# Optimization experiments

Measured on AMD Instinct MI355X. Metric: run time of the kernel, lower is better.

Reference implementation:

```python
import math
import jax, jax.numpy as jnp
import numpy as np

B, N, D, H, NI, NL, NS, MID = 32, 2048, 256, 8, 64, 3, 32, 3


def _ln(x, g, b, eps=1e-5):
    m = jnp.mean(x, axis=-1, keepdims=True)
    v = jnp.mean((x - m) ** 2, axis=-1, keepdims=True)
    return (x - m) * jax.lax.rsqrt(v + eps) * g + b


def _mab(Q, K, mask, Wq, bq, Wk, bk, Wv, bv, Wo, bo, g0, b0, g1, b1):
    # torch's split(dim_split,2)+cat(...,0) == reshape to (B, n, H, dh)
    dh = D // H
    q = (Q @ Wq + bq).reshape(Q.shape[0], Q.shape[1], H, dh)
    k = (K @ Wk + bk).reshape(K.shape[0], K.shape[1], H, dh)
    v = (K @ Wv + bv).reshape(K.shape[0], K.shape[1], H, dh)
    A = jnp.einsum('bqhd,bkhd->bhqk', q, k) / math.sqrt(D)  # note: sqrt(dim_V), faithful
    A = jnp.where(mask[:, None, None, :] == 0, -1e4, A)
    A = jax.nn.softmax(A, axis=-1)
    o = q + jnp.einsum('bhqk,bkhd->bqhd', A, v)
    O = o.reshape(Q.shape[0], Q.shape[1], D)
    O = _ln(O, g0, b0)
    O = O + jax.nn.relu(O @ Wo + bo)
    return _ln(O, g1, b1)


def _forward(x_values, y_target, point_mask, proj_W, proj_b, isab_I,
             isab_Wq, isab_bq, isab_Wk, isab_bk, isab_Wv, isab_bv,
             isab_Wo, isab_bo, isab_g0, isab_b0, isab_g1, isab_b1,
             pma_S, pma_Wq, pma_bq, pma_Wk, pma_bk, pma_Wv, pma_bv,
             pma_Wo, pma_bo, pma_g0, pma_b0, pma_g1, pma_b1):
    # input_dim == max_input_dim, so the zero-padded feature build is a concat
    feats = jnp.concatenate([x_values, y_target[..., None]], axis=-1)  # (B, N, MID+1)
    x = jax.nn.gelu(feats @ proj_W + proj_b, approximate=False)
    ones_mask = jnp.ones((x.shape[0], NI), jnp.float32)
    stk = (isab_Wq, isab_bq, isab_Wk, isab_bk, isab_Wv, isab_bv,
           isab_Wo, isab_bo, isab_g0, isab_b0, isab_g1, isab_b1)
    for l in range(NL):
        I = jnp.broadcast_to(isab_I[l][None], (x.shape[0], NI, D))
        h = _mab(I, x, point_mask, *[a[l, 0] for a in stk])   # mab0: inducing pts attend to X
        x = _mab(x, h, ones_mask, *[a[l, 1] for a in stk])    # mab1: X attends to H (all valid)
    S = jnp.broadcast_to(pma_S[None], (x.shape[0], NS, D))
    return _mab(S, x, point_mask, pma_Wq, pma_bq, pma_Wk, pma_bk, pma_Wv,
                pma_bv, pma_Wo, pma_bo, pma_g0, pma_b0, pma_g1, pma_b1)


def setup_inputs():
    key = jax.random.key(0)
    ks = iter(jax.random.split(key, 40))
    def nrm(shape, s=0.05):
        return jax.random.normal(next(ks), shape, dtype=jnp.float32) * s
    z = lambda shape: jnp.zeros(shape, jnp.float32)
    o = lambda shape: jnp.ones(shape, jnp.float32)
    return {
        'x_values': jax.random.normal(next(ks), (B, N, MID), jnp.float32),
        'y_target': jax.random.normal(next(ks), (B, N), jnp.float32),
        'point_mask': jax.random.randint(next(ks), (B, N), 0, 2).astype(jnp.float32),
        'proj_W': nrm((MID + 1, D)), 'proj_b': z((D,)),
        'isab_I': nrm((NL, NI, D), 0.1),
        'isab_Wq': nrm((NL, 2, D, D)), 'isab_bq': z((NL, 2, D)),
        'isab_Wk': nrm((NL, 2, D, D)), 'isab_bk': z((NL, 2, D)),
        'isab_Wv': nrm((NL, 2, D, D)), 'isab_bv': z((NL, 2, D)),
        'isab_Wo': nrm((NL, 2, D, D)), 'isab_bo': z((NL, 2, D)),
        'isab_g0': o((NL, 2, D)), 'isab_b0': z((NL, 2, D)),
        'isab_g1': o((NL, 2, D)), 'isab_b1': z((NL, 2, D)),
        'pma_S': nrm((NS, D), 0.1),
        'pma_Wq': nrm((D, D)), 'pma_bq': z((D,)),
        'pma_Wk': nrm((D, D)), 'pma_bk': z((D,)),
        'pma_Wv': nrm((D, D)), 'pma_bv': z((D,)),
        'pma_Wo': nrm((D, D)), 'pma_bo': z((D,)),
        'pma_g0': o((D,)), 'pma_b0': z((D,)),
        'pma_g1': o((D,)), 'pma_b1': z((D,)),
    }


def reference(x_values, y_target, point_mask, proj_W, proj_b, isab_I,
              isab_Wq, isab_bq, isab_Wk, isab_bk, isab_Wv, isab_bv,
              isab_Wo, isab_bo, isab_g0, isab_b0, isab_g1, isab_b1,
              pma_S, pma_Wq, pma_bq, pma_Wk, pma_bk, pma_Wv, pma_bv,
              pma_Wo, pma_bo, pma_g0, pma_b0, pma_g1, pma_b1):
    return _forward(x_values, y_target, point_mask, proj_W, proj_b, isab_I,
                    isab_Wq, isab_bq, isab_Wk, isab_bk, isab_Wv, isab_bv,
                    isab_Wo, isab_bo, isab_g0, isab_b0, isab_g1, isab_b1,
                    pma_S, pma_Wq, pma_bq, pma_Wk, pma_bk, pma_Wv, pma_bv,
                    pma_Wo, pma_bo, pma_g0, pma_b0, pma_g1, pma_b1)
```

## Files before the change

### kernel.cpp

```cpp
#include <hip/hip_runtime.h>
#include <hip/hip_bf16.h>


typedef __attribute__((ext_vector_type(8))) short short8;
typedef __attribute__((ext_vector_type(4))) float f32x4;
typedef __attribute__((ext_vector_type(4))) ushort ushort4v;

__device__ __forceinline__ ushort f2bf(float f) {
  uint u = __builtin_bit_cast(uint, f);
  u += 0x7fffu + ((u >> 16) & 1u);
  return (ushort)(u >> 16);
}
__device__ __forceinline__ float bf2f(ushort h) {
  uint u = (uint)h << 16;
  return __builtin_bit_cast(float, u);
}

__global__ __launch_bounds__(256) void prep_weights(
    const float* __restrict__ Wq, const float* __restrict__ Wk,
    const float* __restrict__ Wv, const float* __restrict__ Wo,
    const float* __restrict__ pWq, const float* __restrict__ pWk,
    const float* __restrict__ pWv, const float* __restrict__ pWo,
    ushort* __restrict__ wt)
{
  __shared__ float tile[64][65];
  const int m = blockIdx.y;
  const int t = blockIdx.x;
  const int tr = (t >> 2) * 64;
  const int tc = (t & 3) * 64;
  const float* src;
  if (m < 24) {
    int l = m >> 3, s = (m >> 2) & 1, w = m & 3;
    const float* base = (w == 0) ? Wq : (w == 1) ? Wk : (w == 2) ? Wv : Wo;
    src = base + (size_t)(l * 2 + s) * 65536;
  } else {
    int w = m & 3;
    src = (w == 0) ? pWq : (w == 1) ? pWk : (w == 2) ? pWv : pWo;
  }
  const int tid = threadIdx.x;
  const int cn = tid & 63;
  const int rk = tid >> 6;
#pragma unroll
  for (int j = 0; j < 16; ++j) {
    int kl = rk + j * 4;
    tile[kl][cn] = src[(size_t)(tr + kl) * 256 + tc + cn];
  }
  __syncthreads();
  ushort* dst = wt + (size_t)m * 65536;
#pragma unroll
  for (int j = 0; j < 16; ++j) {
    int nl = rk + j * 4;
    dst[(size_t)(tc + nl) * 256 + tr + cn] = f2bf(tile[cn][nl]);
  }
}

__global__ __launch_bounds__(256) void proj_gelu(
    const float* __restrict__ xv, const float* __restrict__ yt,
    const float* __restrict__ pW, const float* __restrict__ pb,
    ushort* __restrict__ xb)
{
  const int d = threadIdx.x;
  const int row0 = blockIdx.x * 8;
  const float w0 = pW[d], w1 = pW[256 + d], w2 = pW[512 + d], w3 = pW[768 + d];
  const float bz = pb[d];
#pragma unroll
  for (int rr = 0; rr < 8; ++rr) {
    int row = row0 + rr;
    float f0 = xv[(size_t)row * 3 + 0];
    float f1 = xv[(size_t)row * 3 + 1];
    float f2 = xv[(size_t)row * 3 + 2];
    float f3 = yt[row];
    float a = bz + f0 * w0 + f1 * w1 + f2 * w2 + f3 * w3;
    float g = 0.5f * a * (1.f + erff(a * 0.70710678118654752f));
    xb[(size_t)row * 256 + d] = f2bf(g);
  }
}

__global__ __launch_bounds__(256) void gemm_q(
    const float* __restrict__ iI, const float* __restrict__ pS,
    const ushort* __restrict__ wt, const float* __restrict__ ibq,
    const float* __restrict__ pbq, ushort* __restrict__ q_all)
{
  const int bq = blockIdx.x;
  const float* A; const ushort* Wt; const float* bias; ushort* out; int M;
  if (bq < 3) { A = iI + bq * 16384; Wt = wt + (size_t)(bq * 8) * 65536; bias = ibq + bq * 512; out = q_all + bq * 16384; M = 64; }
  else        { A = pS; Wt = wt + (size_t)24 * 65536; bias = pbq; out = q_all + 49152; M = 32; }
  const int tid = threadIdx.x;
  const int wave = tid >> 6, lane = tid & 63;
  const int l15 = lane & 15, l4 = lane >> 4, koff = l4 * 8;
  f32x4 acc[4][4];
#pragma unroll
  for (int i = 0; i < 4; ++i)
#pragma unroll
    for (int j = 0; j < 4; ++j) acc[i][j] = (f32x4)0.f;
#pragma unroll
  for (int ks = 0; ks < 8; ++ks) {
    short8 af[4];
#pragma unroll
    for (int mf = 0; mf < 4; ++mf) {
      if (mf * 16 < M) {
        const float* ap = A + (size_t)(mf * 16 + l15) * 256 + ks * 32 + koff;
        float4 f0 = *(const float4*)ap;
        float4 f1 = *(const float4*)(ap + 4);
        short8 sv;
        sv[0] = (short)f2bf(f0.x); sv[1] = (short)f2bf(f0.y);
        sv[2] = (short)f2bf(f0.z); sv[3] = (short)f2bf(f0.w);
        sv[4] = (short)f2bf(f1.x); sv[5] = (short)f2bf(f1.y);
        sv[6] = (short)f2bf(f1.z); sv[7] = (short)f2bf(f1.w);
        af[mf] = sv;
      } else af[mf] = (short8)0;
    }
#pragma unroll
    for (int nf = 0; nf < 4; ++nf) {
      short8 bf = *(const short8*)(Wt + (size_t)(wave * 64 + nf * 16 + l15) * 256 + ks * 32 + koff);
#pragma unroll
      for (int mf = 0; mf < 4; ++mf)
        acc[mf][nf] = __builtin_amdgcn_mfma_f32_16x16x32_bf16(af[mf], bf, acc[mf][nf], 0, 0, 0);
    }
  }
#pragma unroll
  for (int mf = 0; mf < 4; ++mf) {
    if (mf * 16 >= M) continue;
#pragma unroll
    for (int nf = 0; nf < 4; ++nf) {
      int col = wave * 64 + nf * 16 + l15;
      float bcol = bias[col];
#pragma unroll
      for (int r = 0; r < 4; ++r)
        out[(size_t)(mf * 16 + l4 * 4 + r) * 256 + col] = f2bf(acc[mf][nf][r] + bcol);
    }
  }
}

template <int EPI, bool OUTF32, int COLS>
__global__ __launch_bounds__(COLS * 2, (COLS == 128) ? 4 : 2) void gemm_bp(
    const ushort* __restrict__ A,
    const ushort* __restrict__ Wt0, const ushort* __restrict__ Wt1, const ushort* __restrict__ Wt2,
    const float* __restrict__ b0, const float* __restrict__ b1, const float* __restrict__ b2,
    void* __restrict__ o0, void* __restrict__ o1, void* __restrict__ o2,
    const float* __restrict__ lng, const float* __restrict__ lnb,
    int ny, int nyz)
{
  constexpr int WC = COLS / 64;
  constexpr int PS = COLS * 64;
  constexpr int ROWB = COLS * 2;
  __shared__ __align__(16) char Bs[4 * PS];
  __shared__ float redbuf[(EPI == 3) ? 1280 : 4];
  const int bid = blockIdx.x;
  const int rest = bid >> 3;
  const int yz = rest % nyz;
  const int bx = ((rest / nyz) << 3) | (bid & 7);
  const int y = yz % ny;
  const int z = yz / ny;
  const ushort* Wt = (z == 0) ? Wt0 : ((z == 1) ? Wt1 : Wt2);
  const float* bias = (z == 0) ? b0 : ((z == 1) ? b1 : b2);
  void* outp = (z == 0) ? o0 : ((z == 1) ? o1 : o2);
  const int pcol = y * COLS;

  const int tid = threadIdx.x;
  const int wave = tid >> 6, lane = tid & 63;
  const int wc = wave % WC, wr = wave / WC;
  const int l15 = lane & 15, l4 = lane >> 4;
  const int row0 = bx * 128;
  const int sn = tid >> 1, sseg = tid & 1;

  f32x4 acc[4][4];
#pragma unroll
  for (int i = 0; i < 4; ++i)
#pragma unroll
    for (int j = 0; j < 4; ++j) acc[i][j] = (f32x4)0.f;

#pragma unroll
  for (int half = 0; half < 2; ++half) {
    if (half) __syncthreads();
    {
      const ushort* src = Wt + (size_t)(pcol + sn) * 256 + half * 128 + sseg * 64;
#pragma unroll
      for (int c = 0; c < 8; ++c) {
        uint4 w = *(const uint4*)(src + c * 8);
        int plane = sseg * 2 + (c >> 2);
        char* dst = Bs + plane * PS + sn * 64 + (((c & 3) * 16) ^ (((sn >> 1) & 3) << 4));
        *(uint4*)dst = w;
      }
    }
    __syncthreads();
#pragma unroll
    for (int ks = 0; ks < 4; ++ks) {
      short8 af[4];
#pragma unroll
      for (int mfa = 0; mfa < 4; ++mfa)
        af[mfa] = *(const short8*)(A + (size_t)(row0 + wr * 64 + mfa * 16 + l15) * 256 + half * 128 + ks * 32 + l4 * 8);
#pragma unroll
      for (int nfb = 0; nfb < 4; ++nfb) {
        int n = wc * 64 + nfb * 16 + l15;
        short8 bf = *(const short8*)(Bs + ks * PS + n * 64 + ((l4 * 16) ^ (((n >> 1) & 3) << 4)));
#pragma unroll
        for (int mfa = 0; mfa < 4; ++mfa)
          acc[mfa][nfb] = __builtin_amdgcn_mfma_f32_16x16x32_bf16(bf, af[mfa], acc[mfa][nfb], 0, 0, 0);
      }
    }
  }

  if constexpr (EPI == 0) {
    __syncthreads();
#pragma unroll
    for (int nfb = 0; nfb < 4; ++nfb) {
      f32x4 bv = *(const f32x4*)(bias + pcol + wc * 64 + nfb * 16 + l4 * 4);
      int colb = wc * 128 + nfb * 32 + l4 * 8;
#pragma unroll
      for (int mfa = 0; mfa < 4; ++mfa) {
        int row = wr * 64 + mfa * 16 + l15;
        ushort4v pk;
#pragma unroll
        for (int i = 0; i < 4; ++i) pk[i] = f2bf(acc[mfa][nfb][i] + bv[i]);
        *(ushort4v*)(Bs + row * ROWB + (colb ^ ((row & 7) << 4))) = pk;
      }
    }
    __syncthreads();
    const int srow = tid >> 2, seg = tid & 3;
#pragma unroll
    for (int rr = 0; rr < 2; ++rr) {
      int row = srow + rr * 64;
      int x = (row & 7) << 4;
      ushort* gdst = (ushort*)outp + (size_t)(row0 + row) * 256 + pcol;
#pragma unroll
      for (int it = 0; it < 4; ++it) {
        int colb = seg * 16 + it * 64;
        uint4 v = *(const uint4*)(Bs + row * ROWB + (colb ^ x));
        *(uint4*)(gdst + colb / 2) = v;
      }
    }
  } else {
    float* red1 = redbuf;
    float* red2 = redbuf + 512;
    float* mv_ = redbuf + 1024;
    float* rv_ = redbuf + 1152;
    float s1[4] = {0.f, 0.f, 0.f, 0.f}, s2[4] = {0.f, 0.f, 0.f, 0.f};
#pragma unroll
    for (int nfb = 0; nfb < 4; ++nfb) {
      int col0 = wc * 64 + nfb * 16 + l4 * 4;
      f32x4 bv = *(const f32x4*)(bias + col0);
#pragma unroll
      for (int mfa = 0; mfa < 4; ++mfa) {
        size_t row = (size_t)row0 + wr * 64 + mfa * 16 + l15;
        ushort4v rz = *(const ushort4v*)(A + row * 256 + col0);
#pragma unroll
        for (int i = 0; i < 4; ++i) {
          float zz = bf2f(rz[i]) + fmaxf(acc[mfa][nfb][i] + bv[i], 0.f);
          acc[mfa][nfb][i] = zz;
          s1[mfa] += zz;
          s2[mfa] += zz * zz;
        }
      }
    }
#pragma unroll
    for (int mfa = 0; mfa < 4; ++mfa) {
      s1[mfa] += __shfl_xor(s1[mfa], 16); s1[mfa] += __shfl_xor(s1[mfa], 32);
      s2[mfa] += __shfl_xor(s2[mfa], 16); s2[mfa] += __shfl_xor(s2[mfa], 32);
    }
    if (l4 == 0) {
#pragma unroll
      for (int mfa = 0; mfa < 4; ++mfa) {
        red1[wc * 128 + wr * 64 + mfa * 16 + l15] = s1[mfa];
        red2[wc * 128 + wr * 64 + mfa * 16 + l15] = s2[mfa];
      }
    }
    __syncthreads();
    if (tid < 128) {
      float m1 = red1[tid] + red1[128 + tid] + red1[256 + tid] + red1[384 + tid];
      float m2 = red2[tid] + red2[128 + tid] + red2[256 + tid] + red2[384 + tid];
      float mean = m1 * 0.00390625f;
      float var = m2 * 0.00390625f - mean * mean;
      mv_[tid] = mean;
      rv_[tid] = rsqrtf(var + 1e-5f);
    }
    __syncthreads();
#pragma unroll
    for (int nfb = 0; nfb < 4; ++nfb) {
      int col0 = wc * 64 + nfb * 16 + l4 * 4;
      f32x4 gg = *(const f32x4*)(lng + col0);
      f32x4 bb = *(const f32x4*)(lnb + col0);
      int colb = col0 * 2;
#pragma unroll
      for (int mfa = 0; mfa < 4; ++mfa) {
        int lr = wr * 64 + mfa * 16 + l15;
        float mean = mv_[lr], rs = rv_[lr];
        if constexpr (OUTF32) {
          f32x4 w;
#pragma unroll
          for (int i = 0; i < 4; ++i) w[i] = (acc[mfa][nfb][i] - mean) * rs * gg[i] + bb[i];
          *(f32x4*)((float*)outp + ((size_t)row0 + lr) * 256 + col0) = w;
        } else {
          ushort4v pk;
#pragma unroll
          for (int i = 0; i < 4; ++i) pk[i] = f2bf((acc[mfa][nfb][i] - mean) * rs * gg[i] + bb[i]);
          *(ushort4v*)(Bs + lr * ROWB + (colb ^ ((lr & 7) << 4))) = pk;
        }
      }
    }
    if constexpr (!OUTF32) {
      __syncthreads();
      const int srow = tid >> 2, seg = tid & 3;
      int x = (srow & 7) << 4;
      ushort* gdst = (ushort*)outp + (size_t)(row0 + srow) * 256;
#pragma unroll
      for (int it = 0; it < 8; ++it) {
        int colb = seg * 16 + it * 64;
        uint4 v = *(const uint4*)(Bs + srow * ROWB + (colb ^ x));
        *(uint4*)(gdst + colb / 2) = v;
      }
    }
  }
}

template <int MF>
__global__ __launch_bounds__(512) void attn_big(
    const ushort* __restrict__ qb, const ushort* __restrict__ kb,
    const ushort* __restrict__ vb, const float* __restrict__ mask,
    ushort* __restrict__ O)
{
  __shared__ __align__(16) ushort Ps[8][64][72];
  __shared__ __align__(16) ushort Vt[8][32][72];
  const int h = blockIdx.x, b = blockIdx.y;
  const int tid = threadIdx.x;
  const int w = tid >> 6, lane = tid & 63;
  const int l15 = lane & 15, l4 = lane >> 4;
  const int koff = l4 * 8;
  const int kvbase = b * 2048;

  short8 qf[MF];
#pragma unroll
  for (int mf = 0; mf < MF; ++mf)
    qf[mf] = *(const short8*)(qb + (size_t)(mf * 16 + l15) * 256 + h * 32 + koff);

  f32x4 Oa[MF][2];
  float Mr[MF][4], Lr[MF][4];
#pragma unroll
  for (int mf = 0; mf < MF; ++mf) {
    Oa[mf][0] = (f32x4)0.f; Oa[mf][1] = (f32x4)0.f;
#pragma unroll
    for (int r = 0; r < 4; ++r) { Mr[mf][r] = -1e30f; Lr[mf][r] = 0.f; }
  }

  for (int c = 0; c < 4; ++c) {
    const int kc = w * 256 + c * 64;
    f32x4 S[MF][4];
#pragma unroll
    for (int nf = 0; nf < 4; ++nf) {
      short8 kf = *(const short8*)(kb + (size_t)(kvbase + kc + nf * 16 + l15) * 256 + h * 32 + koff);
#pragma unroll
      for (int mf = 0; mf < MF; ++mf)
        S[mf][nf] = __builtin_amdgcn_mfma_f32_16x16x32_bf16(qf[mf], kf, (f32x4)0.f, 0, 0, 0);
    }
    float mv[4];
#pragma unroll
    for (int nf = 0; nf < 4; ++nf)
      mv[nf] = mask[(size_t)b * 2048 + kc + nf * 16 + l15];
#pragma unroll
    for (int mf = 0; mf < MF; ++mf)
#pragma unroll
      for (int nf = 0; nf < 4; ++nf)
#pragma unroll
        for (int r = 0; r < 4; ++r) {
          float s = S[mf][nf][r] * 0.0625f;
          S[mf][nf][r] = (mv[nf] != 0.f) ? s : -1e4f;
        }
#pragma unroll
    for (int mf = 0; mf < MF; ++mf)
#pragma unroll
      for (int r = 0; r < 4; ++r) {
        float pm = fmaxf(fmaxf(S[mf][0][r], S[mf][1][r]), fmaxf(S[mf][2][r], S[mf][3][r]));
        pm = fmaxf(pm, __shfl_xor(pm, 1));
        pm = fmaxf(pm, __shfl_xor(pm, 2));
        pm = fmaxf(pm, __shfl_xor(pm, 4));
        pm = fmaxf(pm, __shfl_xor(pm, 8));
        float Mnew = fmaxf(Mr[mf][r], pm);
        float corr = __expf(Mr[mf][r] - Mnew);
        Mr[mf][r] = Mnew;
        float rs = 0.f;
#pragma unroll
        for (int nf = 0; nf < 4; ++nf) {
          float p = __expf(S[mf][nf][r] - Mnew);
          S[mf][nf][r] = p;
          rs += p;
        }
        rs += __shfl_xor(rs, 1);
        rs += __shfl_xor(rs, 2);
        rs += __shfl_xor(rs, 4);
        rs += __shfl_xor(rs, 8);
        Lr[mf][r] = Lr[mf][r] * corr + rs;
        Oa[mf][0][r] *= corr;
        Oa[mf][1][r] *= corr;
      }
#pragma unroll
    for (int dblk = 0; dblk < 4; ++dblk) {
      short8 vv = *(const short8*)(vb + (size_t)(kvbase + kc + lane) * 256 + h * 32 + dblk * 8);
#pragma unroll
      for (int j = 0; j < 8; ++j) Vt[w][dblk * 8 + j][lane] = (ushort)vv[j];
    }
#pragma unroll
    for (int mf = 0; mf < MF; ++mf)
#pragma unroll
      for (int nf = 0; nf < 4; ++nf)
#pragma unroll
        for (int r = 0; r < 4; ++r)
          Ps[w][mf * 16 + l4 * 4 + r][nf * 16 + l15] = f2bf(S[mf][nf][r]);
#pragma unroll
    for (int ks = 0; ks < 2; ++ks) {
      short8 pf[MF];
#pragma unroll
      for (int mf = 0; mf < MF; ++mf)
        pf[mf] = *(const short8*)&Ps[w][mf * 16 + l15][ks * 32 + koff];
#pragma unroll
      for (int nf2 = 0; nf2 < 2; ++nf2) {
        short8 vf = *(const short8*)&Vt[w][nf2 * 16 + l15][ks * 32 + koff];
#pragma unroll
        for (int mf = 0; mf < MF; ++mf)
          Oa[mf][nf2] = __builtin_amdgcn_mfma_f32_16x16x32_bf16(pf[mf], vf, Oa[mf][nf2], 0, 0, 0);
      }
    }
  }

  __syncthreads();
  float* Mw = (float*)&Ps[0][0][0];
  float* Lw = Mw + 512;
  float* Ow = Lw + 512;
#pragma unroll
  for (int mf = 0; mf < MF; ++mf)
#pragma unroll
    for (int r = 0; r < 4; ++r) {
      int row = mf * 16 + l4 * 4 + r;
      if (l15 == 0) { Mw[w * 64 + row] = Mr[mf][r]; Lw[w * 64 + row] = Lr[mf][r]; }
#pragma unroll
      for (int nf2 = 0; nf2 < 2; ++nf2)
        Ow[(w * 64 + row) * 33 + nf2 * 16 + l15] = Oa[mf][nf2][r];
    }
  __syncthreads();
  const int NQ = MF * 16;
  int row = tid >> 3, dg = tid & 7;
  if (row < NQ) {
    float mm = -1e30f;
#pragma unroll
    for (int s = 0; s < 8; ++s) mm = fmaxf(mm, Mw[s * 64 + row]);
    float den = 0.f, es[8];
#pragma unroll
    for (int s = 0; s < 8; ++s) {
      es[s] = __expf(Mw[s * 64 + row] - mm);
      den += Lw[s * 64 + row] * es[s];
    }
    float invden = 1.f / den;
    ushort4v pk;
#pragma unroll
    for (int i = 0; i < 4; ++i) {
      int d = dg * 4 + i;
      float num = 0.f;
#pragma unroll
      for (int s = 0; s < 8; ++s) num += Ow[(s * 64 + row) * 33 + d] * es[s];
      float qv = bf2f(qb[(size_t)row * 256 + h * 32 + d]);
      pk[i] = f2bf(qv + num * invden);
    }
    *(ushort4v*)(O + (size_t)(b * NQ + row) * 256 + h * 32 + dg * 4) = pk;
  }
}

__global__ __launch_bounds__(512, 1) void mab1_fused(
    const ushort* __restrict__ xb, const ushort* __restrict__ wq,
    const float* __restrict__ bq,
    const ushort* __restrict__ kb, const ushort* __restrict__ vb,
    const ushort* __restrict__ wo, const float* __restrict__ bo,
    const float* __restrict__ g0, const float* __restrict__ b0v,
    const float* __restrict__ g1, const float* __restrict__ b1v,
    ushort* __restrict__ outb)
{
  __shared__ __align__(16) ushort Qs[8][64][40];
  __shared__ __align__(16) ushort Ps[8][64][72];
  __shared__ __align__(16) ushort Vt[8][32][72];
  __shared__ float red1[8][64], red2[8][64], mv_[64], rv_[64];
  ushort* o_s = &Ps[0][0][0];
  constexpr int OS = 264;

  const int qt = blockIdx.x, b = blockIdx.y;
  const int tid = threadIdx.x;
  const int w = tid >> 6, lane = tid & 63;
  const int l15 = lane & 15, l4 = lane >> 4;
  const int koff = l4 * 8;
  const size_t row0 = (size_t)b * 2048 + qt * 64;
  const int kvbase = b * 64;
  const int h = w;

#pragma unroll
  for (int dblk = 0; dblk < 4; ++dblk) {
    short8 vv = *(const short8*)(vb + (size_t)(kvbase + lane) * 256 + h * 32 + dblk * 8);
#pragma unroll
    for (int j = 0; j < 8; ++j) Vt[w][dblk * 8 + j][lane] = (ushort)vv[j];
  }
  short8 kf[4];
#pragma unroll
  for (int nf = 0; nf < 4; ++nf)
    kf[nf] = *(const short8*)(kb + (size_t)(kvbase + nf * 16 + l15) * 256 + h * 32 + koff);
  short8 wof[2][8];
#pragma unroll
  for (int nfb = 0; nfb < 2; ++nfb) {
    int n = w * 32 + nfb * 16 + l15;
#pragma unroll
    for (int ks = 0; ks < 8; ++ks)
      wof[nfb][ks] = *(const short8*)(wo + (size_t)n * 256 + ks * 32 + koff);
  }

  {
    f32x4 qa[4][2];
#pragma unroll
    for (int i = 0; i < 4; ++i) { qa[i][0] = (f32x4)0.f; qa[i][1] = (f32x4)0.f; }
#pragma unroll
    for (int ks = 0; ks < 8; ++ks) {
      short8 af[4];
#pragma unroll
      for (int mfa = 0; mfa < 4; ++mfa)
        af[mfa] = *(const short8*)(xb + (row0 + mfa * 16 + l15) * 256 + ks * 32 + koff);
#pragma unroll
      for (int nfb = 0; nfb < 2; ++nfb) {
        int n = w * 32 + nfb * 16 + l15;
        short8 bf = *(const short8*)(wq + (size_t)n * 256 + ks * 32 + koff);
#pragma unroll
        for (int mfa = 0; mfa < 4; ++mfa)
          qa[mfa][nfb] = __builtin_amdgcn_mfma_f32_16x16x32_bf16(bf, af[mfa], qa[mfa][nfb], 0, 0, 0);
      }
    }
#pragma unroll
    for (int nfb = 0; nfb < 2; ++nfb) {
      f32x4 bv = *(const f32x4*)(bq + w * 32 + nfb * 16 + l4 * 4);
#pragma unroll
      for (int mfa = 0; mfa < 4; ++mfa) {
        ushort4v pk;
#pragma unroll
        for (int i = 0; i < 4; ++i) pk[i] = f2bf(qa[mfa][nfb][i] + bv[i]);
        *(ushort4v*)&Qs[w][mfa * 16 + l15][nfb * 16 + l4 * 4] = pk;
      }
    }
  }

  short8 qf[4];
#pragma unroll
  for (int mf = 0; mf < 4; ++mf)
    qf[mf] = *(const short8*)&Qs[w][mf * 16 + l15][koff];

  f32x4 S[4][4];
#pragma unroll
  for (int nf = 0; nf < 4; ++nf) {
#pragma unroll
    for (int mf = 0; mf < 4; ++mf)
      S[mf][nf] = __builtin_amdgcn_mfma_f32_16x16x32_bf16(qf[mf], kf[nf], (f32x4)0.f, 0, 0, 0);
  }
  float Lr[4][4];
#pragma unroll
  for (int mf = 0; mf < 4; ++mf)
#pragma unroll
    for (int r = 0; r < 4; ++r) {
      float pm = fmaxf(fmaxf(S[mf][0][r], S[mf][1][r]), fmaxf(S[mf][2][r], S[mf][3][r])) * 0.0625f;
      pm = fmaxf(pm, __shfl_xor(pm, 1));
      pm = fmaxf(pm, __shfl_xor(pm, 2));
      pm = fmaxf(pm, __shfl_xor(pm, 4));
      pm = fmaxf(pm, __shfl_xor(pm, 8));
      float rs = 0.f;
#pragma unroll
      for (int nf = 0; nf < 4; ++nf) {
        float p = __expf(S[mf][nf][r] * 0.0625f - pm);
        S[mf][nf][r] = p;
        rs += p;
      }
      rs += __shfl_xor(rs, 1);
      rs += __shfl_xor(rs, 2);
      rs += __shfl_xor(rs, 4);
      rs += __shfl_xor(rs, 8);
      Lr[mf][r] = rs;
    }
#pragma unroll
  for (int mf = 0; mf < 4; ++mf)
#pragma unroll
    for (int nf = 0; nf < 4; ++nf)
#pragma unroll
      for (int r = 0; r < 4; ++r)
        Ps[w][mf * 16 + l4 * 4 + r][nf * 16 + l15] = f2bf(S[mf][nf][r]);
  f32x4 Oa[4][2];
#pragma unroll
  for (int mf = 0; mf < 4; ++mf) { Oa[mf][0] = (f32x4)0.f; Oa[mf][1] = (f32x4)0.f; }
#pragma unroll
  for (int ks = 0; ks < 2; ++ks) {
    short8 pf[4];
#pragma unroll
    for (int mf = 0; mf < 4; ++mf)
      pf[mf] = *(const short8*)&Ps[w][mf * 16 + l15][ks * 32 + koff];
#pragma unroll
    for (int nf2 = 0; nf2 < 2; ++nf2) {
      short8 vf = *(const short8*)&Vt[w][nf2 * 16 + l15][ks * 32 + koff];
#pragma unroll
      for (int mf = 0; mf < 4; ++mf)
        Oa[mf][nf2] = __builtin_amdgcn_mfma_f32_16x16x32_bf16(pf[mf], vf, Oa[mf][nf2], 0, 0, 0);
    }
  }

  {
    float s1[4][4], s2[4][4];
#pragma unroll
    for (int mf = 0; mf < 4; ++mf)
#pragma unroll
      for (int r = 0; r < 4; ++r) {
        float invL = 1.f / Lr[mf][r];
        s1[mf][r] = 0.f; s2[mf][r] = 0.f;
#pragma unroll
        for (int nf2 = 0; nf2 < 2; ++nf2) {
          float qv = bf2f(Qs[w][mf * 16 + l4 * 4 + r][nf2 * 16 + l15]);
          float z = qv + Oa[mf][nf2][r] * invL;
          Oa[mf][nf2][r] = z;
          s1[mf][r] += z;
          s2[mf][r] += z * z;
        }
#pragma unroll
        for (int off = 1; off < 16; off <<= 1) {
          s1[mf][r] += __shfl_xor(s1[mf][r], off);
          s2[mf][r] += __shfl_xor(s2[mf][r], off);
        }
        if (l15 == 0) {
          int row = mf * 16 + l4 * 4 + r;
          red1[w][row] = s1[mf][r];
          red2[w][row] = s2[mf][r];
        }
      }
  }
  __syncthreads();
  if (tid < 64) {
    float m1 = 0.f, m2 = 0.f;
#pragma unroll
    for (int s = 0; s < 8; ++s) { m1 += red1[s][tid]; m2 += red2[s][tid]; }
    float mean = m1 * 0.00390625f;
    float var = m2 * 0.00390625f - mean * mean;
    mv_[tid] = mean;
    rv_[tid] = rsqrtf(var + 1e-5f);
  }
  __syncthreads();
#pragma unroll
  for (int nf2 = 0; nf2 < 2; ++nf2) {
    int col = h * 32 + nf2 * 16 + l15;
    float gc = g0[col], bc = b0v[col];
#pragma unroll
    for (int mf = 0; mf < 4; ++mf)
#pragma unroll
      for (int r = 0; r < 4; ++r) {
        int row = mf * 16 + l4 * 4 + r;
        float v = (Oa[mf][nf2][r] - mv_[row]) * rv_[row] * gc + bc;
        o_s[row * OS + col] = f2bf(v);
      }
  }
  __syncthreads();

  f32x4 oa[4][2];
#pragma unroll
  for (int i = 0; i < 4; ++i) { oa[i][0] = (f32x4)0.f; oa[i][1] = (f32x4)0.f; }
#pragma unroll
  for (int ks = 0; ks < 8; ++ks) {
    short8 af[4];
#pragma unroll
    for (int mfa = 0; mfa < 4; ++mfa)
      af[mfa] = *(const short8*)&o_s[(mfa * 16 + l15) * OS + ks * 32 + koff];
#pragma unroll
    for (int nfb = 0; nfb < 2; ++nfb) {
#pragma unroll
      for (int mfa = 0; mfa < 4; ++mfa)
        oa[mfa][nfb] = __builtin_amdgcn_mfma_f32_16x16x32_bf16(wof[nfb][ks], af[mfa], oa[mfa][nfb], 0, 0, 0);
    }
  }
  float t1[4] = {0.f, 0.f, 0.f, 0.f}, t2[4] = {0.f, 0.f, 0.f, 0.f};
#pragma unroll
  for (int nfb = 0; nfb < 2; ++nfb) {
    int col0 = w * 32 + nfb * 16 + l4 * 4;
    f32x4 bv = *(const f32x4*)(bo + col0);
#pragma unroll
    for (int mfa = 0; mfa < 4; ++mfa) {
      int row = mfa * 16 + l15;
      ushort4v rz = *(const ushort4v*)&o_s[row * OS + col0];
#pragma unroll
      for (int i = 0; i < 4; ++i) {
        float zz = bf2f(rz[i]) + fmaxf(oa[mfa][nfb][i] + bv[i], 0.f);
        oa[mfa][nfb][i] = zz;
        t1[mfa] += zz;
        t2[mfa] += zz * zz;
      }
    }
  }
#pragma unroll
  for (int mfa = 0; mfa < 4; ++mfa) {
    t1[mfa] += __shfl_xor(t1[mfa], 16); t1[mfa] += __shfl_xor(t1[mfa], 32);
    t2[mfa] += __shfl_xor(t2[mfa], 16); t2[mfa] += __shfl_xor(t2[mfa], 32);
  }
  if (l4 == 0) {
#pragma unroll
    for (int mfa = 0; mfa < 4; ++mfa) {
      red1[w][mfa * 16 + l15] = t1[mfa];
      red2[w][mfa * 16 + l15] = t2[mfa];
    }
  }
  __syncthreads();
  if (tid < 64) {
    float m1 = 0.f, m2 = 0.f;
#pragma unroll
    for (int s = 0; s < 8; ++s) { m1 += red1[s][tid]; m2 += red2[s][tid]; }
    float mean = m1 * 0.00390625f;
    float var = m2 * 0.00390625f - mean * mean;
    mv_[tid] = mean;
    rv_[tid] = rsqrtf(var + 1e-5f);
  }
  __syncthreads();
#pragma unroll
  for (int nfb = 0; nfb < 2; ++nfb) {
    int col0 = w * 32 + nfb * 16 + l4 * 4;
    f32x4 gg = *(const f32x4*)(g1 + col0);
    f32x4 bb = *(const f32x4*)(b1v + col0);
#pragma unroll
    for (int mfa = 0; mfa < 4; ++mfa) {
      int row = mfa * 16 + l15;
      ushort4v pk;
#pragma unroll
      for (int i = 0; i < 4; ++i)
        pk[i] = f2bf((oa[mfa][nfb][i] - mv_[row]) * rv_[row] * gg[i] + bb[i]);
      *(ushort4v*)&o_s[row * OS + col0] = pk;
    }
  }
  __syncthreads();
  {
    const int r_ = tid >> 3, sg = tid & 7;
    ushort* gdst = outb + (row0 + r_) * 256 + sg * 32;
    const ushort* src = &o_s[r_ * OS + sg * 32];
#pragma unroll
    for (int it = 0; it < 4; ++it) {
      uint4 v = *(const uint4*)(src + it * 8);
      *(uint4*)(gdst + it * 8) = v;
    }
  }
}

__global__ __launch_bounds__(256) void ln4(
    const ushort* __restrict__ in, ushort* __restrict__ out,
    const float* __restrict__ g, const float* __restrict__ bb)
{
  const int w = threadIdx.x >> 6, lane = threadIdx.x & 63;
  const size_t row = (size_t)blockIdx.x * 4 + w;
  ushort4v u = *(const ushort4v*)(in + row * 256 + lane * 4);
  float v[4];
#pragma unroll
  for (int i = 0; i < 4; ++i) v[i] = bf2f(u[i]);
  float s1 = v[0] + v[1] + v[2] + v[3];
  float s2 = v[0] * v[0] + v[1] * v[1] + v[2] * v[2] + v[3] * v[3];
#pragma unroll
  for (int off = 1; off < 64; off <<= 1) {
    s1 += __shfl_xor(s1, off);
    s2 += __shfl_xor(s2, off);
  }
  float mean = s1 * 0.00390625f;
  float var = s2 * 0.00390625f - mean * mean;
  float rs = rsqrtf(var + 1e-5f);
  f32x4 gg = *(const f32x4*)(g + lane * 4);
  f32x4 bv = *(const f32x4*)(bb + lane * 4);
  ushort4v p;
#pragma unroll
  for (int i = 0; i < 4; ++i) p[i] = f2bf((v[i] - mean) * rs * gg[i] + bv[i]);
  *(ushort4v*)(out + row * 256 + lane * 4) = p;
}

extern "C" void kernel_launch(void* const* d_in, const int* in_sizes, int n_in,
                              void* d_out, int out_size, void* d_ws, size_t ws_size,
                              hipStream_t stream) {
  const float* xv = (const float*)d_in[0];
  const float* yt = (const float*)d_in[1];
  const float* pmask = (const float*)d_in[2];
  const float* prW = (const float*)d_in[3];
  const float* prb = (const float*)d_in[4];
  const float* iI = (const float*)d_in[5];
  const float* iWq = (const float*)d_in[6];
  const float* ibq = (const float*)d_in[7];
  const float* iWk = (const float*)d_in[8];
  const float* ibk = (const float*)d_in[9];
  const float* iWv = (const float*)d_in[10];
  const float* ibv = (const float*)d_in[11];
  const float* iWo = (const float*)d_in[12];
  const float* ibo = (const float*)d_in[13];
  const float* ig0 = (const float*)d_in[14];
  const float* ib0 = (const float*)d_in[15];
  const float* ig1 = (const float*)d_in[16];
  const float* ib1 = (const float*)d_in[17];
  const float* pS = (const float*)d_in[18];
  const float* pWq = (const float*)d_in[19];
  const float* pbq = (const float*)d_in[20];
  const float* pWk = (const float*)d_in[21];
  const float* pbk = (const float*)d_in[22];
  const float* pWv = (const float*)d_in[23];
  const float* pbv = (const float*)d_in[24];
  const float* pWo = (const float*)d_in[25];
  const float* pbo = (const float*)d_in[26];
  const float* pg0 = (const float*)d_in[27];
  const float* pb0 = (const float*)d_in[28];
  const float* pg1 = (const float*)d_in[29];
  const float* pb1 = (const float*)d_in[30];

  char* ws = (char*)d_ws;
  if (ws_size < 172621824u) return;
  ushort* xb = (ushort*)(ws + 0);
  ushort* ob = (ushort*)(ws + 33554432);
  ushort* hb = (ushort*)(ws + 67108864);
  ushort* kbw = (ushort*)(ws + 101711872);
  ushort* vbw = (ushort*)(ws + 135266304);
  ushort* wt = (ushort*)(ws + 168820736);
  ushort* q_all = (ushort*)(ws + 172490752);

  prep_weights<<<dim3(16, 28), 256, 0, stream>>>(iWq, iWk, iWv, iWo, pWq, pWk, pWv, pWo, wt);
  proj_gelu<<<8192, 256, 0, stream>>>(xv, yt, prW, prb, xb);
  gemm_q<<<4, 256, 0, stream>>>(iI, pS, wt, ibq, pbq, q_all);

  for (int l = 0; l < 3; ++l) {
    const int s0 = l * 2, s1 = l * 2 + 1;
    const ushort* wk = wt + (size_t)(l * 8 + 1) * 65536;
    const ushort* wv = wt + (size_t)(l * 8 + 2) * 65536;
    const ushort* wo0 = wt + (size_t)(l * 8 + 3) * 65536;
    const ushort* wq1 = wt + (size_t)(l * 8 + 4) * 65536;
    const ushort* wk1 = wt + (size_t)(l * 8 + 5) * 65536;
    const ushort* wv1 = wt + (size_t)(l * 8 + 6) * 65536;
    const ushort* wo1 = wt + (size_t)(l * 8 + 7) * 65536;
    gemm_bp<0, false, 128><<<2048, 256, 0, stream>>>(
        xb, wk, wv, wv, ibk + s0 * 256, ibv + s0 * 256, ibv + s0 * 256,
        kbw, vbw, vbw, nullptr, nullptr, 2, 4);
    attn_big<4><<<dim3(8, 32), 512, 0, stream>>>(q_all + l * 16384, kbw, vbw, pmask, ob);
    ln4<<<512, 256, 0, stream>>>(ob, ob, ig0 + s0 * 256, ib0 + s0 * 256);
    gemm_bp<3, false, 256><<<16, 512, 0, stream>>>(
        ob, wo0, wo0, wo0, ibo + s0 * 256, ibo + s0 * 256, ibo + s0 * 256,
        hb, hb, hb, ig1 + s0 * 256, ib1 + s0 * 256, 1, 1);
    gemm_bp<0, false, 128><<<64, 256, 0, stream>>>(
        hb, wk1, wv1, wv1, ibk + s1 * 256, ibv + s1 * 256, ibv + s1 * 256,
        kbw, vbw, vbw, nullptr, nullptr, 2, 4);
    mab1_fused<<<dim3(32, 32), 512, 0, stream>>>(
        xb, wq1, ibq + s1 * 256, kbw, vbw, wo1, ibo + s1 * 256,
        ig0 + s1 * 256, ib0 + s1 * 256, ig1 + s1 * 256, ib1 + s1 * 256, xb);
  }
  gemm_bp<0, false, 128><<<2048, 256, 0, stream>>>(
      xb, wt + (size_t)25 * 65536, wt + (size_t)26 * 65536, wt + (size_t)26 * 65536,
      pbk, pbv, pbv, kbw, vbw, vbw, nullptr, nullptr, 2, 4);
  attn_big<2><<<dim3(8, 32), 512, 0, stream>>>(q_all + 49152, kbw, vbw, pmask, ob);
  ln4<<<256, 256, 0, stream>>>(ob, ob, pg0, pb0);
  gemm_bp<3, true, 256><<<8, 512, 0, stream>>>(
      ob, wt + (size_t)27 * 65536, wt + (size_t)27 * 65536, wt + (size_t)27 * 65536,
      pbo, pbo, pbo, d_out, d_out, d_out, pg1, pb1, 1, 1);
}
```

Measured before the change: 853.0 us.

## Shrink mab1 LDS and register footprint to allow multiple blocks per CU

```diff
diff --git a/kernel.cpp b/kernel.cpp
--- a/kernel.cpp
+++ b/kernel.cpp
@@ -463,7 +463,7 @@
   }
 }
 
-__global__ __launch_bounds__(512, 1) void mab1_fused(
+__global__ __launch_bounds__(512, 4) void mab1_fused(
     const ushort* __restrict__ xb, const ushort* __restrict__ wq,
     const float* __restrict__ bq,
     const ushort* __restrict__ kb, const ushort* __restrict__ vb,
@@ -473,10 +473,10 @@
     ushort* __restrict__ outb)
 {
   __shared__ __align__(16) ushort Qs[8][64][40];
-  __shared__ __align__(16) ushort Ps[8][64][72];
-  __shared__ __align__(16) ushort Vt[8][32][72];
+  __shared__ __align__(16) ushort Psh[8][16][40];
+  __shared__ __align__(16) ushort Vth[8][32][40];
   __shared__ float red1[8][64], red2[8][64], mv_[64], rv_[64];
-  ushort* o_s = &Ps[0][0][0];
+  ushort* o_s = &Qs[0][0][0];
   constexpr int OS = 264;
 
   const int qt = blockIdx.x, b = blockIdx.y;
@@ -488,23 +488,23 @@
   const int kvbase = b * 64;
   const int h = w;
 
-#pragma unroll
-  for (int dblk = 0; dblk < 4; ++dblk) {
-    short8 vv = *(const short8*)(vb + (size_t)(kvbase + lane) * 256 + h * 32 + dblk * 8);
-#pragma unroll
-    for (int j = 0; j < 8; ++j) Vt[w][dblk * 8 + j][lane] = (ushort)vv[j];
-  }
   short8 kf[4];
 #pragma unroll
   for (int nf = 0; nf < 4; ++nf)
     kf[nf] = *(const short8*)(kb + (size_t)(kvbase + nf * 16 + l15) * 256 + h * 32 + koff);
-  short8 wof[2][8];
-#pragma unroll
-  for (int nfb = 0; nfb < 2; ++nfb) {
-    int n = w * 32 + nfb * 16 + l15;
-#pragma unroll
-    for (int ks = 0; ks < 8; ++ks)
-      wof[nfb][ks] = *(const short8*)(wo + (size_t)n * 256 + ks * 32 + koff);
+  const int key = lane & 31, dh2 = lane >> 5;
+  short8 vvB0, vvB1;
+  {
+    const ushort* vsrcA = vb + (size_t)(kvbase + key) * 256 + h * 32 + dh2 * 16;
+    const ushort* vsrcB = vb + (size_t)(kvbase + 32 + key) * 256 + h * 32 + dh2 * 16;
+    short8 vvA0 = *(const short8*)vsrcA;
+    short8 vvA1 = *(const short8*)(vsrcA + 8);
+    vvB0 = *(const short8*)vsrcB;
+    vvB1 = *(const short8*)(vsrcB + 8);
+#pragma unroll
+    for (int j = 0; j < 8; ++j) Vth[w][dh2 * 16 + j][key] = (ushort)vvA0[j];
+#pragma unroll
+    for (int j = 0; j < 8; ++j) Vth[w][dh2 * 16 + 8 + j][key] = (ushort)vvA1[j];
   }
 
   {
@@ -574,28 +574,40 @@
       rs += __shfl_xor(rs, 8);
       Lr[mf][r] = rs;
     }
-#pragma unroll
-  for (int mf = 0; mf < 4; ++mf)
-#pragma unroll
-    for (int nf = 0; nf < 4; ++nf)
+
+  f32x4 Oa[4][2];
+#pragma unroll
+  for (int mf = 0; mf < 4; ++mf) { Oa[mf][0] = (f32x4)0.f; Oa[mf][1] = (f32x4)0.f; }
+#pragma unroll
+  for (int mf = 0; mf < 4; ++mf) {
+#pragma unroll
+    for (int nf = 0; nf < 2; ++nf)
 #pragma unroll
       for (int r = 0; r < 4; ++r)
-        Ps[w][mf * 16 + l4 * 4 + r][nf * 16 + l15] = f2bf(S[mf][nf][r]);
-  f32x4 Oa[4][2];
-#pragma unroll
-  for (int mf = 0; mf < 4; ++mf) { Oa[mf][0] = (f32x4)0.f; Oa[mf][1] = (f32x4)0.f; }
-#pragma unroll
-  for (int ks = 0; ks < 2; ++ks) {
-    short8 pf[4];
-#pragma unroll
-    for (int mf = 0; mf < 4; ++mf)
-      pf[mf] = *(const short8*)&Ps[w][mf * 16 + l15][ks * 32 + koff];
+        Psh[w][l4 * 4 + r][nf * 16 + l15] = f2bf(S[mf][nf][r]);
+    short8 pf = *(const short8*)&Psh[w][l15][koff];
 #pragma unroll
     for (int nf2 = 0; nf2 < 2; ++nf2) {
-      short8 vf = *(const short8*)&Vt[w][nf2 * 16 + l15][ks * 32 + koff];
-#pragma unroll
-      for (int mf = 0; mf < 4; ++mf)
-        Oa[mf][nf2] = __builtin_amdgcn_mfma_f32_16x16x32_bf16(pf[mf], vf, Oa[mf][nf2], 0, 0, 0);
+      short8 vf = *(const short8*)&Vth[w][nf2 * 16 + l15][koff];
+      Oa[mf][nf2] = __builtin_amdgcn_mfma_f32_16x16x32_bf16(pf, vf, Oa[mf][nf2], 0, 0, 0);
+    }
+  }
+#pragma unroll
+  for (int j = 0; j < 8; ++j) Vth[w][dh2 * 16 + j][key] = (ushort)vvB0[j];
+#pragma unroll
+  for (int j = 0; j < 8; ++j) Vth[w][dh2 * 16 + 8 + j][key] = (ushort)vvB1[j];
+#pragma unroll
+  for (int mf = 0; mf < 4; ++mf) {
+#pragma unroll
+    for (int nf = 0; nf < 2; ++nf)
+#pragma unroll
+      for (int r = 0; r < 4; ++r)
+        Psh[w][l4 * 4 + r][nf * 16 + l15] = f2bf(S[mf][nf + 2][r]);
+    short8 pf = *(const short8*)&Psh[w][l15][koff];
+#pragma unroll
+    for (int nf2 = 0; nf2 < 2; ++nf2) {
+      short8 vf = *(const short8*)&Vth[w][nf2 * 16 + l15][koff];
+      Oa[mf][nf2] = __builtin_amdgcn_mfma_f32_16x16x32_bf16(pf, vf, Oa[mf][nf2], 0, 0, 0);
     }
   }
 
@@ -664,9 +676,11 @@
       af[mfa] = *(const short8*)&o_s[(mfa * 16 + l15) * OS + ks * 32 + koff];
 #pragma unroll
     for (int nfb = 0; nfb < 2; ++nfb) {
+      int n = w * 32 + nfb * 16 + l15;
+      short8 bf = *(const short8*)(wo + (size_t)n * 256 + ks * 32 + koff);
 #pragma unroll
       for (int mfa = 0; mfa < 4; ++mfa)
-        oa[mfa][nfb] = __builtin_amdgcn_mfma_f32_16x16x32_bf16(wof[nfb][ks], af[mfa], oa[mfa][nfb], 0, 0, 0);
+        oa[mfa][nfb] = __builtin_amdgcn_mfma_f32_16x16x32_bf16(bf, af[mfa], oa[mfa][nfb], 0, 0, 0);
     }
   }
   float t1[4] = {0.f, 0.f, 0.f, 0.f}, t2[4] = {0.f, 0.f, 0.f, 0.f};
```

After: 799.5 us. 1.07x faster.
